# Optimization experiments

Measured on AMD Instinct MI355X. Metric: run time of the kernel, lower is better.

## Reference

```python
import jax, jax.numpy as jnp
import numpy as np

EPS = 1e-08
COS_ID_THRESH = 0.9999
L_SH, R_SH, NECK = 11, 12, 0


def setup_inputs() -> dict:
    key = jax.random.key(0)
    landmarks = jax.random.normal(key, (32768, 543, 3), dtype=jnp.float32)
    return {"landmarks": landmarks}


def reference(landmarks):
    # landmarks: (T, N, 3)
    ls = landmarks[:, L_SH]            # (T, 3)
    rs = landmarks[:, R_SH]            # (T, 3)
    neck = landmarks[:, NECK]          # (T, 3)

    sv = rs - ls                       # shoulder vector, (T, 3)
    s = jnp.linalg.norm(sv, axis=-1) + EPS          # per-frame scale, (T,)

    # project shoulder vector to xz-plane and normalize
    sxz = sv * jnp.array([1.0, 0.0, 1.0], dtype=sv.dtype)
    sxz = sxz / (jnp.linalg.norm(sxz, axis=-1, keepdims=True) + EPS)

    # cos of angle to target [1,0,0] is just the x component
    cos_t = jnp.clip(sxz[:, 0], -1.0, 1.0)          # (T,)
    sin_t = jnp.sqrt(jnp.clip(1.0 - cos_t * cos_t, 0.0, None))

    # Rodrigues for fixed axis (0,1,0): K and K@K are constants
    K = jnp.array([[0.0, 0.0, 1.0],
                   [0.0, 0.0, 0.0],
                   [-1.0, 0.0, 0.0]], dtype=landmarks.dtype)
    K2 = K @ K                                       # diag(-1, 0, -1)
    I3 = jnp.eye(3, dtype=landmarks.dtype)

    R = I3 + sin_t[:, None, None] * K + (1.0 - cos_t)[:, None, None] * K2  # (T,3,3)
    R = jnp.where((jnp.abs(cos_t) > COS_ID_THRESH)[:, None, None], I3, R)

    centered = landmarks - neck[:, None, :]          # (T, N, 3)
    # rotated[t] = centered[t] @ R[t].T
    rotated = jnp.einsum('tnj,tij->tni', centered, R)
    return rotated / s[:, None, None]
```

## Files before the change

### kernel.cpp

```cpp
#include <hip/hip_runtime.h>
#include <math.h>

#define N_LM 543
#define ROW (N_LM * 3)
#define L_SH 11
#define R_SH 12

__global__ __launch_bounds__(256)
void sim3_kernel(const float* __restrict__ in, float* __restrict__ out) {
    const int t = blockIdx.x;
    const float* __restrict__ row = in + (size_t)t * ROW;
    float* __restrict__ orow = out + (size_t)t * ROW;

    const float nx = row[0], ny = row[1], nz = row[2];
    const float lsx = row[L_SH * 3 + 0], lsy = row[L_SH * 3 + 1], lsz = row[L_SH * 3 + 2];
    const float rsx = row[R_SH * 3 + 0], rsy = row[R_SH * 3 + 1], rsz = row[R_SH * 3 + 2];

    const float svx = rsx - lsx;
    const float svy = rsy - lsy;
    const float svz = rsz - lsz;

    const float s = sqrtf(svx * svx + svy * svy + svz * svz) + 1e-8f;
    const float inv_s = 1.0f / s;

    const float sxz_n = sqrtf(svx * svx + svz * svz) + 1e-8f;
    float c = svx / sxz_n;
    c = fminf(fmaxf(c, -1.0f), 1.0f);
    float st = sqrtf(fmaxf(1.0f - c * c, 0.0f));

    if (fabsf(c) > 0.9999f) { c = 1.0f; st = 0.0f; }

    for (int n = threadIdx.x; n < N_LM; n += blockDim.x) {
        const int o = n * 3;
        const float x = row[o + 0] - nx;
        const float y = row[o + 1] - ny;
        const float z = row[o + 2] - nz;
        orow[o + 0] = (c * x + st * z) * inv_s;
        orow[o + 1] = y * inv_s;
        orow[o + 2] = (-st * x + c * z) * inv_s;
    }
}

extern "C" void kernel_launch(void* const* d_in, const int* in_sizes, int n_in,
                              void* d_out, int out_size, void* d_ws, size_t ws_size,
                              hipStream_t stream) {
    const float* in = (const float*)d_in[0];
    float* out = (float*)d_out;
    const int T = in_sizes[0] / ROW;
    sim3_kernel<<<T, 256, 0, stream>>>(in, out);
}
```

Before: 345.1 us.

## Flatten to per-thread float4 chunks spanning frames with per-frame parameter recompute

Replaces the one-block-per-frame kernel with a flat grid where each thread loads three float4 vectors (four landmarks) and writes three float4 vectors. Each thread recomputes the rotation, scale and neck offset for the one or two frames its chunk covers, selecting per landmark. This targets the strided scalar accesses and the idle threads in the old per-frame loop (543 landmarks over 256 threads). In exchange it adds redundant parameter loads and math per thread. It also has no tail handling, so it assumes the total element count is a multiple of 3072.

```diff
diff --git a/kernel.cpp b/kernel.cpp
--- a/kernel.cpp
+++ b/kernel.cpp
@@ -2,43 +2,69 @@
 #include <math.h>
 
 #define N_LM 543
-#define ROW (N_LM * 3)
-#define L_SH 11
-#define R_SH 12
+#define ROW 1629
 
-__global__ __launch_bounds__(256)
-void sim3_kernel(const float* __restrict__ in, float* __restrict__ out) {
-    const int t = blockIdx.x;
-    const float* __restrict__ row = in + (size_t)t * ROW;
-    float* __restrict__ orow = out + (size_t)t * ROW;
-
-    const float nx = row[0], ny = row[1], nz = row[2];
-    const float lsx = row[L_SH * 3 + 0], lsy = row[L_SH * 3 + 1], lsz = row[L_SH * 3 + 2];
-    const float rsx = row[R_SH * 3 + 0], rsy = row[R_SH * 3 + 1], rsz = row[R_SH * 3 + 2];
-
+__device__ __forceinline__ void row_params(const float* __restrict__ in, unsigned t,
+                                           float& c, float& st, float& inv_s,
+                                           float& nx, float& ny, float& nz) {
+    const float* row = in + (size_t)t * ROW;
+    nx = row[0]; ny = row[1]; nz = row[2];
+    const float lsx = row[33], lsy = row[34], lsz = row[35];
+    const float rsx = row[36], rsy = row[37], rsz = row[38];
     const float svx = rsx - lsx;
     const float svy = rsy - lsy;
     const float svz = rsz - lsz;
+    const float s = sqrtf(svx*svx + svy*svy + svz*svz) + 1e-8f;
+    inv_s = 1.0f / s;
+    const float sxz_n = sqrtf(svx*svx + svz*svz) + 1e-8f;
+    c = svx / sxz_n;
+    c = fminf(fmaxf(c, -1.0f), 1.0f);
+    st = sqrtf(fmaxf(1.0f - c*c, 0.0f));
+    if (fabsf(c) > 0.9999f) { c = 1.0f; st = 0.0f; }
+}
 
-    const float s = sqrtf(svx * svx + svy * svy + svz * svz) + 1e-8f;
-    const float inv_s = 1.0f / s;
+__global__ __launch_bounds__(256)
+void sim3_vec(const float4* __restrict__ in4, float4* __restrict__ out4,
+              const float* __restrict__ in) {
+    const unsigned i = blockIdx.x * 256u + threadIdx.x;
+    const size_t q = (size_t)i * 3u;
 
-    const float sxz_n = sqrtf(svx * svx + svz * svz) + 1e-8f;
-    float c = svx / sxz_n;
-    c = fminf(fmaxf(c, -1.0f), 1.0f);
-    float st = sqrtf(fmaxf(1.0f - c * c, 0.0f));
+    const float4 a = in4[q + 0];
+    const float4 b = in4[q + 1];
+    const float4 d = in4[q + 2];
+    const float f[12] = {a.x, a.y, a.z, a.w, b.x, b.y, b.z, b.w, d.x, d.y, d.z, d.w};
 
-    if (fabsf(c) > 0.9999f) { c = 1.0f; st = 0.0f; }
+    const unsigned P0 = 4u * i;
+    const unsigned t0 = P0 / 543u;
+    const unsigned t3 = (P0 + 3u) / 543u;
 
-    for (int n = threadIdx.x; n < N_LM; n += blockDim.x) {
-        const int o = n * 3;
-        const float x = row[o + 0] - nx;
-        const float y = row[o + 1] - ny;
-        const float z = row[o + 2] - nz;
-        orow[o + 0] = (c * x + st * z) * inv_s;
-        orow[o + 1] = y * inv_s;
-        orow[o + 2] = (-st * x + c * z) * inv_s;
+    float c0, st0, is0, nx0, ny0, nz0;
+    row_params(in, t0, c0, st0, is0, nx0, ny0, nz0);
+    float c1 = c0, st1 = st0, is1 = is0, nx1 = nx0, ny1 = ny0, nz1 = nz0;
+    unsigned split = 4u;
+    if (t3 != t0) {
+        row_params(in, t3, c1, st1, is1, nx1, ny1, nz1);
+        split = t3 * 543u - P0;
     }
+
+    float o[12];
+#pragma unroll
+    for (int j = 0; j < 4; ++j) {
+        const bool hi = (unsigned)j >= split;
+        const float c  = hi ? c1  : c0;
+        const float st = hi ? st1 : st0;
+        const float is = hi ? is1 : is0;
+        const float x = f[3*j + 0] - (hi ? nx1 : nx0);
+        const float y = f[3*j + 1] - (hi ? ny1 : ny0);
+        const float z = f[3*j + 2] - (hi ? nz1 : nz0);
+        o[3*j + 0] = ( c  * x + st * z) * is;
+        o[3*j + 1] =   y * is;
+        o[3*j + 2] = (-st * x + c  * z) * is;
+    }
+
+    out4[q + 0] = make_float4(o[0], o[1], o[2],  o[3]);
+    out4[q + 1] = make_float4(o[4], o[5], o[6],  o[7]);
+    out4[q + 2] = make_float4(o[8], o[9], o[10], o[11]);
 }
 
 extern "C" void kernel_launch(void* const* d_in, const int* in_sizes, int n_in,
@@ -46,6 +72,7 @@
                               hipStream_t stream) {
     const float* in = (const float*)d_in[0];
     float* out = (float*)d_out;
-    const int T = in_sizes[0] / ROW;
-    sim3_kernel<<<T, 256, 0, stream>>>(in, out);
+    const int total_threads = in_sizes[0] / 12;
+    const int blocks = total_threads / 256;
+    sim3_vec<<<blocks, 256, 0, stream>>>((const float4*)in, (float4*)out, in);
 }
```

Measured after the change: 349.4 us. Within noise of the previous version (+1.3%).
